# Kernel optimization log

Hardware: AMD Instinct MI355X
Metric: run time of the kernel (lower is better)

## Reference

```python
import jax, jax.numpy as jnp
import numpy as np

B, T, V, E, H, D1 = 4096, 255, 32000, 64, 64, 32

def setup_inputs() -> dict:
    key = jax.random.key(0)
    ks = jax.random.split(key, 6)
    return {
        "input_diffs": jax.random.randint(ks[0], (B, T), 0, V, dtype=jnp.int32),
        "embeddings": jax.random.normal(ks[1], (V, E), dtype=jnp.float32) * 0.1,
        "Wx": jax.random.normal(ks[2], (E, 4 * H), dtype=jnp.float32) * 0.1,
        "Wh": jax.random.normal(ks[3], (H, 4 * H), dtype=jnp.float32) * 0.1,
        "b_lstm": jnp.zeros((4 * H,), dtype=jnp.float32),
        "W1": jax.random.normal(ks[4], (E, D1), dtype=jnp.float32) * 0.1,
        "b1": jnp.zeros((D1,), dtype=jnp.float32),
        "W2": jax.random.normal(ks[5], (D1, V), dtype=jnp.float32) * 0.02,
        "b2": jnp.zeros((V,), dtype=jnp.float32),
    }

def _lstm_last(emb, Wx, Wh, b):
    # emb: [B, T, E] -> scan over time; Keras gate order i, f, c(g), o
    h0 = jnp.zeros((emb.shape[0], H), dtype=emb.dtype)
    c0 = jnp.zeros_like(h0)
    def step(carry, xt):
        h, c = carry
        z = xt @ Wx + h @ Wh + b                    # [B, 4H]
        i, f, g, o = jnp.split(z, 4, axis=-1)
        i = jax.nn.sigmoid(i); f = jax.nn.sigmoid(f)
        g = jnp.tanh(g);       o = jax.nn.sigmoid(o)
        c = f * c + i * g
        h = o * jnp.tanh(c)
        return (h, c), None
    (h, _), _ = jax.lax.scan(step, (h0, c0), jnp.swapaxes(emb, 0, 1))
    return h  # [B, H] (return_sequences=False)

def reference(input_diffs, embeddings, Wx, Wh, b_lstm, W1, b1, W2, b2):
    emb = embeddings[input_diffs]                   # [B, T, E] embedding lookup
    h = _lstm_last(emb, Wx, Wh, b_lstm)             # [B, H]
    out = jax.nn.relu(h @ W1 + b1)                  # [B, 32]
    logits = out @ W2 + b2                          # [B, V]
    return jax.nn.softmax(logits, axis=-1)
```

## Files before the change

### kernel.cpp

```cpp
#include <hip/hip_runtime.h>
#include <hip/hip_bf16.h>

#define B_  4096
#define T_  255
#define V_  32000
#define E_  64
#define H_  64
#define D1_ 32

#define NCT           2000
#define NCHUNK        10
#define CT_PER_CHUNK  200
#define CT_PER_WAVE   50

typedef __attribute__((ext_vector_type(8))) short bf16x8;
typedef __attribute__((ext_vector_type(4))) float f32x4;

__device__ __forceinline__ ushort f2bf(float f) {
    __hip_bfloat16 h = __float2bfloat16(f);
    return *reinterpret_cast<ushort*>(&h);
}
__device__ __forceinline__ float fast_sigmoid(float x) {
    return __builtin_amdgcn_rcpf(1.f + __expf(-x));
}
__device__ __forceinline__ float fast_tanh_pre(float y) {
    return 1.f - 2.f * __builtin_amdgcn_rcpf(1.f + __expf(y));
}
__device__ __forceinline__ float fast_tanh(float x) {
    return 1.f - 2.f * __builtin_amdgcn_rcpf(1.f + __expf(2.f * x));
}

__device__ __forceinline__ int hswz(int row, int colb) {
    return row * 128 + (colb ^ ((row & 7) << 4));
}

__global__ __launch_bounds__(256)
void prep_kernel(const float* __restrict__ emb, ushort* __restrict__ emb_bf,
                 const float* __restrict__ W2,  ushort* __restrict__ w2p)
{
    if (blockIdx.x < 1000) {
        int i = blockIdx.x * 256 + threadIdx.x;
        const float4 a = ((const float4*)emb)[i * 2];
        const float4 b = ((const float4*)emb)[i * 2 + 1];
        ushort t[8] = { f2bf(a.x), f2bf(a.y), f2bf(a.z), f2bf(a.w),
                        f2bf(b.x), f2bf(b.y), f2bf(b.z), f2bf(b.w) };
        *(ushort4*)(&emb_bf[i * 8])     = *(ushort4*)(&t[0]);
        *(ushort4*)(&emb_bf[i * 8 + 4]) = *(ushort4*)(&t[4]);
    } else {
        int t = (blockIdx.x - 1000) * 256 + threadIdx.x;
        if (t >= NCT * 64) return;
        int ct = t >> 6, l = t & 63;
        int kbase = (l >> 4) * 8, c = ct * 16 + (l & 15);
        ushort tmp[8];
        #pragma unroll
        for (int i = 0; i < 8; ++i)
            tmp[i] = f2bf(W2[(kbase + i) * V_ + c]);
        *(ushort4*)(&w2p[t * 8])     = *(ushort4*)(&tmp[0]);
        *(ushort4*)(&w2p[t * 8 + 4]) = *(ushort4*)(&tmp[4]);
    }
}

__global__ __launch_bounds__(256)
void lstm_mfma_kernel(const int* __restrict__ idx,
                      const ushort* __restrict__ emb_bf,
                      const float* __restrict__ Wx,
                      const float* __restrict__ Wh,
                      const float* __restrict__ b,
                      const float* __restrict__ W1,
                      const float* __restrict__ b1,
                      ushort* __restrict__ out32bf)
{
    __shared__ __align__(16) char hbuf[2][2048];
    __shared__ int idxs[16 * 257];

    const int tid  = threadIdx.x;
    const int lane = tid & 63;
    const int w    = tid >> 6;
    const int r0   = blockIdx.x * 16;
    const int lrow = lane & 15;
    const int lhi  = lane >> 4;
    const int jcol = w * 16 + lrow;

    bf16x8 bw[16];
    f32x4 bsp[4];
    #pragma unroll
    for (int g = 0; g < 4; ++g) {
        const int col = g * 64 + jcol;
        const float sc = (g == 2) ? 2.f : 1.f;
        const float bv = b[col] * sc;
        bsp[g] = (f32x4){bv, bv, bv, bv};
        #pragma unroll
        for (int s = 0; s < 4; ++s) {
            bf16x8 f;
            #pragma unroll
            for (int i = 0; i < 8; ++i) {
                int k = s * 32 + lhi * 8 + i;
                float v = (k < 64) ? Wx[k * 256 + col] : Wh[(k - 64) * 256 + col];
                f[i] = (short)f2bf(v * sc);
            }
            bw[g * 4 + s] = f;
        }
    }

    bf16x8 bw1[2];
    float b1v = 0.f;
    if (w < 2) {
        const int col = w * 16 + lrow;
        b1v = b1[col];
        #pragma unroll
        for (int s = 0; s < 2; ++s) {
            bf16x8 f;
            #pragma unroll
            for (int i = 0; i < 8; ++i)
                f[i] = (short)f2bf(W1[(s * 32 + lhi * 8 + i) * D1_ + col]);
            bw1[s] = f;
        }
    }

    {
        const int row = tid >> 4, tc = tid & 15;
        #pragma unroll
        for (int k = 0; k < 16; ++k) {
            int t = k * 16 + tc;
            if (t < T_) idxs[row * 257 + t] = idx[(r0 + row) * T_ + t];
        }
        ((float2*)hbuf[0])[tid] = make_float2(0.f, 0.f);
    }
    __syncthreads();

    bf16x8 xe0, xe1, xo0, xo1;
    {
        int iv = idxs[lrow * 257 + 0];
        xe0 = *(const bf16x8*)(emb_bf + iv * 64 + lhi * 8);
        xe1 = *(const bf16x8*)(emb_bf + iv * 64 + 32 + lhi * 8);
        iv = idxs[lrow * 257 + 1];
        xo0 = *(const bf16x8*)(emb_bf + iv * 64 + lhi * 8);
        xo1 = *(const bf16x8*)(emb_bf + iv * 64 + 32 + lhi * 8);
    }

    float cst[4]  = {0.f, 0.f, 0.f, 0.f};

    auto do_step = [&](int t, bf16x8& x0, bf16x8& x1) {
        const int p = t & 1;
        bf16x8 ah2 = *(const bf16x8*)(&hbuf[p][hswz(lrow, lhi * 16)]);
        bf16x8 ah3 = *(const bf16x8*)(&hbuf[p][hswz(lrow, 64 + lhi * 16)]);

        f32x4 z[4];
        #pragma unroll
        for (int g = 0; g < 4; ++g)
            z[g] = __builtin_amdgcn_mfma_f32_16x16x32_bf16(x0, bw[g * 4 + 0], bsp[g], 0, 0, 0);
        #pragma unroll
        for (int g = 0; g < 4; ++g)
            z[g] = __builtin_amdgcn_mfma_f32_16x16x32_bf16(x1, bw[g * 4 + 1], z[g], 0, 0, 0);
        #pragma unroll
        for (int g = 0; g < 4; ++g)
            z[g] = __builtin_amdgcn_mfma_f32_16x16x32_bf16(ah2, bw[g * 4 + 2], z[g], 0, 0, 0);
        #pragma unroll
        for (int g = 0; g < 4; ++g)
            z[g] = __builtin_amdgcn_mfma_f32_16x16x32_bf16(ah3, bw[g * 4 + 3], z[g], 0, 0, 0);

        if (t + 2 < T_) {
            int iv = idxs[lrow * 257 + (t + 2)];
            x0 = *(const bf16x8*)(emb_bf + iv * 64 + lhi * 8);
            x1 = *(const bf16x8*)(emb_bf + iv * 64 + 32 + lhi * 8);
        }

        #pragma unroll
        for (int r = 0; r < 4; ++r) {
            float cn = fast_sigmoid(z[1][r]) * cst[r]
                     + fast_sigmoid(z[0][r]) * fast_tanh_pre(z[2][r]);
            cst[r] = cn;
            float hn = fast_sigmoid(z[3][r]) * fast_tanh(cn);
            const int row = lhi * 4 + r;
            *(ushort*)(&hbuf[p ^ 1][hswz(row, 2 * jcol)]) = f2bf(hn);
        }

        asm volatile("s_waitcnt lgkmcnt(0)\n\ts_barrier" ::: "memory");
    };

    for (int t = 0; t + 1 < T_; t += 2) {
        do_step(t,     xe0, xe1);
        do_step(t + 1, xo0, xo1);
    }
    do_step(T_ - 1, xe0, xe1);

    if (w < 2) {
        bf16x8 e0 = *(const bf16x8*)(&hbuf[1][hswz(lrow, lhi * 16)]);
        bf16x8 e1 = *(const bf16x8*)(&hbuf[1][hswz(lrow, 64 + lhi * 16)]);
        f32x4 zz = (f32x4){b1v, b1v, b1v, b1v};
        zz = __builtin_amdgcn_mfma_f32_16x16x32_bf16(e0, bw1[0], zz, 0, 0, 0);
        zz = __builtin_amdgcn_mfma_f32_16x16x32_bf16(e1, bw1[1], zz, 0, 0, 0);
        #pragma unroll
        for (int r = 0; r < 4; ++r)
            out32bf[(r0 + lhi * 4 + r) * D1_ + w * 16 + lrow] =
                f2bf(fmaxf(zz[r], 0.f));
    }
}

template <int PASS>
__global__ __launch_bounds__(256)
void head2_mfma_kernel(const ushort* __restrict__ out32bf,
                       const ushort* __restrict__ w2p,
                       const float* __restrict__ b2,
                       float* __restrict__ partial,
                       float* __restrict__ out)
{
    __shared__ float red[4][16];
    __shared__ float sinvs[16];

    const int tid  = threadIdx.x;
    const int lane = tid & 63;
    const int w    = tid >> 6;
    const int lrow = lane & 15;
    const int lhi  = lane >> 4;
    const int r0    = blockIdx.x * 16;
    const int chunk = blockIdx.y;

    if (PASS == 2) {
        if (tid < 16) {
            float s = 0.f;
            #pragma unroll
            for (int c = 0; c < NCHUNK; ++c) s += partial[(r0 + tid) * NCHUNK + c];
            sinvs[tid] = 1.f / s;
        }
        __syncthreads();
    }

    const bf16x8 A = *(const bf16x8*)(out32bf + (r0 + lrow) * D1_ + lhi * 8);

    float sacc[4] = {0.f, 0.f, 0.f, 0.f};
    float si[4];
    if (PASS == 2) {
        #pragma unroll
        for (int r = 0; r < 4; ++r) si[r] = sinvs[lhi * 4 + r];
    }

    const int ct0 = chunk * CT_PER_CHUNK + w * CT_PER_WAVE;
    for (int i = 0; i < CT_PER_WAVE; ++i) {
        const int ct = ct0 + i;
        const bf16x8 Bf = *(const bf16x8*)(w2p + ct * 512 + lane * 8);
        f32x4 z = __builtin_amdgcn_mfma_f32_16x16x32_bf16(A, Bf, (f32x4){0.f, 0.f, 0.f, 0.f}, 0, 0, 0);
        const float b2v = b2[ct * 16 + lrow];
        #pragma unroll
        for (int r = 0; r < 4; ++r) {
            float e = __expf(z[r] + b2v);
            if (PASS == 1) sacc[r] += e;
            else out[(size_t)(r0 + lhi * 4 + r) * V_ + ct * 16 + lrow] = e * si[r];
        }
    }

    if (PASS == 1) {
        #pragma unroll
        for (int r = 0; r < 4; ++r) {
            float v = sacc[r];
            #pragma unroll
            for (int off = 1; off < 16; off <<= 1) v += __shfl_xor(v, off, 16);
            if (lrow == 0) red[w][lhi * 4 + r] = v;
        }
        __syncthreads();
        if (tid < 16)
            partial[(r0 + tid) * NCHUNK + chunk] =
                red[0][tid] + red[1][tid] + red[2][tid] + red[3][tid];
    }
}

extern "C" void kernel_launch(void* const* d_in, const int* in_sizes, int n_in,
                              void* d_out, int out_size, void* d_ws, size_t ws_size,
                              hipStream_t stream)
{
    (void)in_sizes; (void)n_in; (void)out_size; (void)ws_size;

    const int*   idx = (const int*)  d_in[0];
    const float* emb = (const float*)d_in[1];
    const float* Wx  = (const float*)d_in[2];
    const float* Wh  = (const float*)d_in[3];
    const float* bl  = (const float*)d_in[4];
    const float* W1  = (const float*)d_in[5];
    const float* b1  = (const float*)d_in[6];
    const float* W2  = (const float*)d_in[7];
    const float* b2  = (const float*)d_in[8];
    float* out = (float*)d_out;

    float*  ws      = (float*)d_ws;
    ushort* out32bf = (ushort*)ws;
    ushort* w2p     = (ushort*)(ws + 65536);
    float*  part    = ws + 65536 + 512000;
    ushort* emb_bf  = (ushort*)(ws + 65536 + 512000 + 40960);

    prep_kernel<<<1500, 256, 0, stream>>>(emb, emb_bf, W2, w2p);
    lstm_mfma_kernel<<<256, 256, 0, stream>>>(idx, emb_bf, Wx, Wh, bl, W1, b1, out32bf);

    dim3 g3(B_ / 16, NCHUNK);
    head2_mfma_kernel<1><<<g3, 256, 0, stream>>>(out32bf, w2p, b2, part, out);
    head2_mfma_kernel<2><<<g3, 256, 0, stream>>>(out32bf, w2p, b2, part, out);
}
```

Measured before the change: 338.9 us.

## Halve LSTM rows per block, deepen embedding prefetch, fold log2e into exp2

The LSTM kernel now gives each block 8 batch rows instead of 16 and launches twice as many blocks, with launch bounds asking for two blocks per CU. The intent is to let two independent serial recurrences share a CU and hide each other's MFMA, transcendental and barrier latency. The cost is that the 16-row MFMA tile now holds each row twice, so half the matrix work is redundant. Embedding prefetch depth goes from 2 to 4 timesteps. The log2(e) factor is folded into the gate weights, biases and W2 so that sigmoid, tanh and the softmax exp can call exp2 directly and skip one multiply each.

Result: slower. 381.6 us (+12.6%).

```diff
diff --git a/kernel.cpp b/kernel.cpp
--- a/kernel.cpp
+++ b/kernel.cpp
@@ -13,21 +13,20 @@
 #define CT_PER_CHUNK  200
 #define CT_PER_WAVE   50
 
+#define LOG2E  1.4426950408889634f
+
+#if __has_builtin(__builtin_amdgcn_exp2f)
+#define EXP2F __builtin_amdgcn_exp2f
+#else
+#define EXP2F exp2f
+#endif
+
 typedef __attribute__((ext_vector_type(8))) short bf16x8;
 typedef __attribute__((ext_vector_type(4))) float f32x4;
 
 __device__ __forceinline__ ushort f2bf(float f) {
     __hip_bfloat16 h = __float2bfloat16(f);
     return *reinterpret_cast<ushort*>(&h);
-}
-__device__ __forceinline__ float fast_sigmoid(float x) {
-    return __builtin_amdgcn_rcpf(1.f + __expf(-x));
-}
-__device__ __forceinline__ float fast_tanh_pre(float y) {
-    return 1.f - 2.f * __builtin_amdgcn_rcpf(1.f + __expf(y));
-}
-__device__ __forceinline__ float fast_tanh(float x) {
-    return 1.f - 2.f * __builtin_amdgcn_rcpf(1.f + __expf(2.f * x));
 }
 
 __device__ __forceinline__ int hswz(int row, int colb) {
@@ -54,13 +53,13 @@
         ushort tmp[8];
         #pragma unroll
         for (int i = 0; i < 8; ++i)
-            tmp[i] = f2bf(W2[(kbase + i) * V_ + c]);
+            tmp[i] = f2bf(W2[(kbase + i) * V_ + c] * LOG2E);
         *(ushort4*)(&w2p[t * 8])     = *(ushort4*)(&tmp[0]);
         *(ushort4*)(&w2p[t * 8 + 4]) = *(ushort4*)(&tmp[4]);
     }
 }
 
-__global__ __launch_bounds__(256)
+__global__ __launch_bounds__(256, 2)
 void lstm_mfma_kernel(const int* __restrict__ idx,
                       const ushort* __restrict__ emb_bf,
                       const float* __restrict__ Wx,
@@ -71,12 +70,12 @@
                       ushort* __restrict__ out32bf)
 {
     __shared__ __align__(16) char hbuf[2][2048];
-    __shared__ int idxs[16 * 257];
+    __shared__ int idxs[8 * 257];
 
     const int tid  = threadIdx.x;
     const int lane = tid & 63;
     const int w    = tid >> 6;
-    const int r0   = blockIdx.x * 16;
+    const int r0   = blockIdx.x * 8;
     const int lrow = lane & 15;
     const int lhi  = lane >> 4;
     const int jcol = w * 16 + lrow;
@@ -86,7 +85,7 @@
     #pragma unroll
     for (int g = 0; g < 4; ++g) {
         const int col = g * 64 + jcol;
-        const float sc = (g == 2) ? 2.f : 1.f;
+        const float sc = (g == 2) ? (2.f * LOG2E) : (-LOG2E);
         const float bv = b[col] * sc;
         bsp[g] = (f32x4){bv, bv, bv, bv};
         #pragma unroll
@@ -118,24 +117,31 @@
     }
 
     {
-        const int row = tid >> 4, tc = tid & 15;
-        #pragma unroll
-        for (int k = 0; k < 16; ++k) {
-            int t = k * 16 + tc;
+        const int row = tid >> 5, tc = tid & 31;
+        #pragma unroll
+        for (int k = 0; k < 8; ++k) {
+            int t = k * 32 + tc;
             if (t < T_) idxs[row * 257 + t] = idx[(r0 + row) * T_ + t];
         }
         ((float2*)hbuf[0])[tid] = make_float2(0.f, 0.f);
     }
     __syncthreads();
 
-    bf16x8 xe0, xe1, xo0, xo1;
+    const int grow = lrow & 7;
+    bf16x8 xa0, xa1, xb0, xb1, xc0, xc1, xd0, xd1;
     {
-        int iv = idxs[lrow * 257 + 0];
-        xe0 = *(const bf16x8*)(emb_bf + iv * 64 + lhi * 8);
-        xe1 = *(const bf16x8*)(emb_bf + iv * 64 + 32 + lhi * 8);
-        iv = idxs[lrow * 257 + 1];
-        xo0 = *(const bf16x8*)(emb_bf + iv * 64 + lhi * 8);
-        xo1 = *(const bf16x8*)(emb_bf + iv * 64 + 32 + lhi * 8);
+        int iv = idxs[grow * 257 + 0];
+        xa0 = *(const bf16x8*)(emb_bf + iv * 64 + lhi * 8);
+        xa1 = *(const bf16x8*)(emb_bf + iv * 64 + 32 + lhi * 8);
+        iv = idxs[grow * 257 + 1];
+        xb0 = *(const bf16x8*)(emb_bf + iv * 64 + lhi * 8);
+        xb1 = *(const bf16x8*)(emb_bf + iv * 64 + 32 + lhi * 8);
+        iv = idxs[grow * 257 + 2];
+        xc0 = *(const bf16x8*)(emb_bf + iv * 64 + lhi * 8);
+        xc1 = *(const bf16x8*)(emb_bf + iv * 64 + 32 + lhi * 8);
+        iv = idxs[grow * 257 + 3];
+        xd0 = *(const bf16x8*)(emb_bf + iv * 64 + lhi * 8);
+        xd1 = *(const bf16x8*)(emb_bf + iv * 64 + 32 + lhi * 8);
     }
 
     float cst[4]  = {0.f, 0.f, 0.f, 0.f};
@@ -159,18 +165,22 @@
         for (int g = 0; g < 4; ++g)
             z[g] = __builtin_amdgcn_mfma_f32_16x16x32_bf16(ah3, bw[g * 4 + 3], z[g], 0, 0, 0);
 
-        if (t + 2 < T_) {
-            int iv = idxs[lrow * 257 + (t + 2)];
+        if (t + 4 < T_) {
+            int iv = idxs[grow * 257 + (t + 4)];
             x0 = *(const bf16x8*)(emb_bf + iv * 64 + lhi * 8);
             x1 = *(const bf16x8*)(emb_bf + iv * 64 + 32 + lhi * 8);
         }
 
         #pragma unroll
         for (int r = 0; r < 4; ++r) {
-            float cn = fast_sigmoid(z[1][r]) * cst[r]
-                     + fast_sigmoid(z[0][r]) * fast_tanh_pre(z[2][r]);
+            float si = __builtin_amdgcn_rcpf(1.f + EXP2F(z[0][r]));
+            float sf = __builtin_amdgcn_rcpf(1.f + EXP2F(z[1][r]));
+            float tg = 1.f - 2.f * __builtin_amdgcn_rcpf(1.f + EXP2F(z[2][r]));
+            float cn = sf * cst[r] + si * tg;
             cst[r] = cn;
-            float hn = fast_sigmoid(z[3][r]) * fast_tanh(cn);
+            float so = __builtin_amdgcn_rcpf(1.f + EXP2F(z[3][r]));
+            float th = 1.f - 2.f * __builtin_amdgcn_rcpf(1.f + EXP2F(cn * (2.f * LOG2E)));
+            float hn = so * th;
             const int row = lhi * 4 + r;
             *(ushort*)(&hbuf[p ^ 1][hswz(row, 2 * jcol)]) = f2bf(hn);
         }
@@ -178,11 +188,15 @@
         asm volatile("s_waitcnt lgkmcnt(0)\n\ts_barrier" ::: "memory");
     };
 
-    for (int t = 0; t + 1 < T_; t += 2) {
-        do_step(t,     xe0, xe1);
-        do_step(t + 1, xo0, xo1);
-    }
-    do_step(T_ - 1, xe0, xe1);
+    for (int t = 0; t + 3 < T_; t += 4) {
+        do_step(t,     xa0, xa1);
+        do_step(t + 1, xb0, xb1);
+        do_step(t + 2, xc0, xc1);
+        do_step(t + 3, xd0, xd1);
+    }
+    do_step(252, xa0, xa1);
+    do_step(253, xb0, xb1);
+    do_step(254, xc0, xc1);
 
     if (w < 2) {
         bf16x8 e0 = *(const bf16x8*)(&hbuf[1][hswz(lrow, lhi * 16)]);
@@ -190,10 +204,12 @@
         f32x4 zz = (f32x4){b1v, b1v, b1v, b1v};
         zz = __builtin_amdgcn_mfma_f32_16x16x32_bf16(e0, bw1[0], zz, 0, 0, 0);
         zz = __builtin_amdgcn_mfma_f32_16x16x32_bf16(e1, bw1[1], zz, 0, 0, 0);
-        #pragma unroll
-        for (int r = 0; r < 4; ++r)
-            out32bf[(r0 + lhi * 4 + r) * D1_ + w * 16 + lrow] =
-                f2bf(fmaxf(zz[r], 0.f));
+        if (lhi < 2) {
+            #pragma unroll
+            for (int r = 0; r < 4; ++r)
+                out32bf[(r0 + lhi * 4 + r) * D1_ + w * 16 + lrow] =
+                    f2bf(fmaxf(zz[r], 0.f));
+        }
     }
 }
 
@@ -240,10 +256,10 @@
         const int ct = ct0 + i;
         const bf16x8 Bf = *(const bf16x8*)(w2p + ct * 512 + lane * 8);
         f32x4 z = __builtin_amdgcn_mfma_f32_16x16x32_bf16(A, Bf, (f32x4){0.f, 0.f, 0.f, 0.f}, 0, 0, 0);
-        const float b2v = b2[ct * 16 + lrow];
+        const float b2s = b2[ct * 16 + lrow] * LOG2E;
         #pragma unroll
         for (int r = 0; r < 4; ++r) {
-            float e = __expf(z[r] + b2v);
+            float e = EXP2F(z[r] + b2s);
             if (PASS == 1) sacc[r] += e;
             else out[(size_t)(r0 + lhi * 4 + r) * V_ + ct * 16 + lrow] = e * si[r];
         }
@@ -288,7 +304,7 @@
     ushort* emb_bf  = (ushort*)(ws + 65536 + 512000 + 40960);
 
     prep_kernel<<<1500, 256, 0, stream>>>(emb, emb_bf, W2, w2p);
-    lstm_mfma_kernel<<<256, 256, 0, stream>>>(idx, emb_bf, Wx, Wh, bl, W1, b1, out32bf);
+    lstm_mfma_kernel<<<B_ / 8, 256, 0, stream>>>(idx, emb_bf, Wx, Wh, bl, W1, b1, out32bf);
 
     dim3 g3(B_ / 16, NCHUNK);
     head2_mfma_kernel<1><<<g3, 256, 0, stream>>>(out32bf, w2p, b2, part, out);
```
